# Kernel tuning notes

Measured on AMD Instinct MI355X. Metric: run time of the kernel, lower is better.

## Reference

```python
import jax, jax.numpy as jnp
import numpy as np

EPS = 1e-12  # torch F.normalize default eps

def setup_inputs() -> dict:
    key = jax.random.key(0)
    k1, k2, k3 = jax.random.split(key, 3)
    B, C, H, W = 32, 512, 64, 64
    HEADS = 8
    local_feature = jax.random.normal(k1, (B, C, H, W), dtype=jnp.float32)
    global_feature = jax.random.normal(k2, (B, C, H, W), dtype=jnp.float32)
    temperature = jnp.ones((HEADS, 1, 1), dtype=jnp.float32)
    proj_w = jax.random.normal(k3, (C, C), dtype=jnp.float32) * 0.02  # project_out 1x1 conv weight [out,in]
    return {"local_feature": local_feature, "global_feature": global_feature,
            "temperature": temperature, "proj_w": proj_w}

def _l2norm(x):
    # F.normalize(x, dim=-1): x / max(||x||_2, eps)
    n = jnp.sqrt(jnp.sum(x * x, axis=-1, keepdims=True))
    return x / jnp.maximum(n, EPS)

def reference(local_feature, global_feature, temperature, proj_w):
    B, C, H, W = local_feature.shape
    heads = temperature.shape[0]
    d = C // heads
    split = lambda x: x.reshape(B, heads, d, H * W)  # b (head c) h w -> b head c (hw)
    q = _l2norm(split(local_feature))
    k = _l2norm(split(global_feature))
    v = split(global_feature)
    # channel-attention: [b,h,d,d] score matrix (d small), softmax over last dim
    attn = jax.nn.softmax(jnp.einsum('bhcn,bhdn->bhcd', q, k) * temperature, axis=-1)
    out = jnp.einsum('bhcd,bhdn->bhcn', attn, v).reshape(B, C, H, W)
    # project_out: 1x1 conv, no bias -> channel GEMM
    return jnp.einsum('oc,bchw->bohw', proj_w, out)
```

## Files before the change

kernel.cpp:

```cpp
#include <hip/hip_runtime.h>
#include <stdint.h>

#define B_N 32
#define C_N 512
#define HEADS_N 8
#define D_N 64
#define N_SP 4096

typedef __attribute__((ext_vector_type(8))) short short8;
typedef __attribute__((ext_vector_type(4))) float f32x4;

__device__ __forceinline__ unsigned int f2bf1(float x) {
  unsigned int u = __float_as_uint(x);
  return (u + 0x7fffu + ((u >> 16) & 1u)) >> 16;
}
__device__ __forceinline__ unsigned int packbf(float lo, float hi) {
  return f2bf1(lo) | (f2bf1(hi) << 16);
}

__global__ __launch_bounds__(256) void attn_partial_kernel(
    const float* __restrict__ localf, const float* __restrict__ globf,
    float* __restrict__ pS, float* __restrict__ pssq, int splitk)
{
  const int h = blockIdx.x, b = blockIdx.y, chunk = blockIdx.z;
  const int t = threadIdx.x;
  const int lane = t & 63, w = t >> 6;
  const int rquad = t >> 4;
  const int c4 = t & 15;

  __shared__ unsigned short tA[64 * 72];
  __shared__ unsigned short tB[64 * 72];
  __shared__ float ssqP[2 * 64 * 16];

  const float* Qb = localf + ((size_t)(b * C_N + h * D_N)) * N_SP;
  const float* Kb = globf  + ((size_t)(b * C_N + h * D_N)) * N_SP;

  const int iters = 64 / splitk;
  const int it0 = chunk * iters;

  f32x4 acc[2][2];
#pragma unroll
  for (int i = 0; i < 2; ++i)
#pragma unroll
    for (int j = 0; j < 2; ++j) acc[i][j] = (f32x4){0.f, 0.f, 0.f, 0.f};

  float ssqA[4] = {0.f, 0.f, 0.f, 0.f}, ssqB[4] = {0.f, 0.f, 0.f, 0.f};
  f32x4 qa[4], ka[4];

  {
    int n0 = it0 * 64 + c4 * 4;
#pragma unroll
    for (int i = 0; i < 4; ++i) {
      int row = i * 16 + rquad;
      qa[i] = *(const f32x4*)(Qb + (size_t)row * N_SP + n0);
      ka[i] = *(const f32x4*)(Kb + (size_t)row * N_SP + n0);
    }
  }

  const int lr = lane & 15, lq = lane >> 4;
  const int rbase = (w >> 1) * 32, cbase = (w & 1) * 32;

  for (int it = it0; it < it0 + iters; ++it) {
#pragma unroll
    for (int i = 0; i < 4; ++i) {
      int row = i * 16 + rquad;
      f32x4 q = qa[i], k = ka[i];
      ssqA[i] += q[0]*q[0] + q[1]*q[1] + q[2]*q[2] + q[3]*q[3];
      ssqB[i] += k[0]*k[0] + k[1]*k[1] + k[2]*k[2] + k[3]*k[3];
      uint2 qp; qp.x = packbf(q[0], q[1]); qp.y = packbf(q[2], q[3]);
      uint2 kp; kp.x = packbf(k[0], k[1]); kp.y = packbf(k[2], k[3]);
      *(uint2*)(tA + row * 72 + c4 * 4) = qp;
      *(uint2*)(tB + row * 72 + c4 * 4) = kp;
    }
    __syncthreads();
    if (it + 1 < it0 + iters) {
      int n0 = (it + 1) * 64 + c4 * 4;
#pragma unroll
      for (int i = 0; i < 4; ++i) {
        int row = i * 16 + rquad;
        qa[i] = *(const f32x4*)(Qb + (size_t)row * N_SP + n0);
        ka[i] = *(const f32x4*)(Kb + (size_t)row * N_SP + n0);
      }
    }
#pragma unroll
    for (int s = 0; s < 2; ++s) {
      short8 af[2], bf[2];
#pragma unroll
      for (int mt = 0; mt < 2; ++mt)
        af[mt] = *(const short8*)(tA + (rbase + mt * 16 + lr) * 72 + (s * 4 + lq) * 8);
#pragma unroll
      for (int nt = 0; nt < 2; ++nt)
        bf[nt] = *(const short8*)(tB + (cbase + nt * 16 + lr) * 72 + (s * 4 + lq) * 8);
#pragma unroll
      for (int mt = 0; mt < 2; ++mt)
#pragma unroll
        for (int nt = 0; nt < 2; ++nt)
          acc[mt][nt] = __builtin_amdgcn_mfma_f32_16x16x32_bf16(
              af[mt], bf[nt], acc[mt][nt], 0, 0, 0);
    }
    __syncthreads();
  }

#pragma unroll
  for (int i = 0; i < 4; ++i) {
    ssqP[(0 * 64 + i * 16 + rquad) * 16 + c4] = ssqA[i];
    ssqP[(1 * 64 + i * 16 + rquad) * 16 + c4] = ssqB[i];
  }
  __syncthreads();

  const size_t obase = (size_t)(b * HEADS_N + h) * (size_t)splitk + chunk;
  if (t < 128) {
    int side = t >> 6, row = t & 63;
    float s = 0.f;
#pragma unroll
    for (int j = 0; j < 16; ++j) s += ssqP[(side * 64 + row) * 16 + j];
    pssq[obase * 128 + t] = s;
  }

  float* ps = pS + obase * 4096;
#pragma unroll
  for (int mt = 0; mt < 2; ++mt)
#pragma unroll
    for (int nt = 0; nt < 2; ++nt)
#pragma unroll
      for (int r = 0; r < 4; ++r) {
        int rg = rbase + mt * 16 + lq * 4 + r;
        int cg = cbase + nt * 16 + lr;
        ps[rg * 64 + cg] = acc[mt][nt][r];
      }
}

__global__ __launch_bounds__(256) void attn_combine_kernel(
    const float* __restrict__ pS, const float* __restrict__ pssq,
    const float* __restrict__ temp, float* __restrict__ attn_out, int splitk)
{
  const int h = blockIdx.x, b = blockIdx.y, t = threadIdx.x;
  __shared__ float S[64 * 68];
  __shared__ float invv[128];

  const size_t base = (size_t)(b * HEADS_N + h) * (size_t)splitk;

  float r[16];
#pragma unroll
  for (int i = 0; i < 16; ++i) r[i] = 0.f;
  for (int c = 0; c < splitk; ++c) {
    const float* p = pS + (base + c) * 4096;
#pragma unroll
    for (int i = 0; i < 16; ++i) r[i] += p[t + 256 * i];
  }
  if (t < 128) {
    float s = 0.f;
    for (int c = 0; c < splitk; ++c) s += pssq[(base + c) * 128 + t];
    invv[t] = 1.0f / fmaxf(sqrtf(s), 1e-12f);
  }
#pragma unroll
  for (int i = 0; i < 16; ++i) {
    int e = t + 256 * i;
    S[(e >> 6) * 68 + (e & 63)] = r[i];
  }
  __syncthreads();

  const float tval = temp[h];
#pragma unroll
  for (int i = 0; i < 16; ++i) {
    int e = t + 256 * i;
    int rw = e >> 6, cl = e & 63;
    S[rw * 68 + cl] *= invv[rw] * invv[64 + cl] * tval;
  }
  __syncthreads();

  if (t < 64) {
    float mx = -1e30f;
#pragma unroll 8
    for (int j = 0; j < 64; ++j) mx = fmaxf(mx, S[t * 68 + j]);
    float sum = 0.f;
#pragma unroll 8
    for (int j = 0; j < 64; ++j) {
      float e = __expf(S[t * 68 + j] - mx);
      S[t * 68 + j] = e;
      sum += e;
    }
    float inv = 1.0f / sum;
    float* op = attn_out + ((size_t)((b * HEADS_N + h) * 64 + t)) * 64;
#pragma unroll 8
    for (int j = 0; j < 64; ++j) op[j] = S[t * 68 + j] * inv;
  }
}

__global__ __launch_bounds__(256) void fold_kernel(
    const float* __restrict__ proj, const float* __restrict__ attn,
    unsigned short* __restrict__ Mout)
{
  const int h = blockIdx.x, b = blockIdx.y, zh = blockIdx.z;
  const int t = threadIdx.x;
  __shared__ float A_[64 * 64];
  const float* ap = attn + (size_t)(b * HEADS_N + h) * 4096;
#pragma unroll
  for (int i = 0; i < 16; ++i) A_[i * 256 + t] = ap[i * 256 + t];
  __syncthreads();
  const int e = t & 63, w = t >> 6;
  float col[64];
#pragma unroll
  for (int cc = 0; cc < 64; ++cc) col[cc] = A_[cc * 64 + e];
  unsigned short* mb = Mout + (size_t)b * C_N * C_N + (size_t)h * 64 + e;
  for (int i = 0; i < 16; ++i) {
    int o = zh * 64 + i * 4 + w;
    const float* pr = proj + (size_t)o * C_N + h * 64;
    float s = 0.f;
#pragma unroll
    for (int cc = 0; cc < 64; cc += 4) {
      f32x4 p = *(const f32x4*)(pr + cc);
      s += p[0]*col[cc] + p[1]*col[cc+1] + p[2]*col[cc+2] + p[3]*col[cc+3];
    }
    mb[(size_t)o * C_N] = (unsigned short)f2bf1(s);
  }
}

__global__ __launch_bounds__(256, 2) void final_gemm_kernel(
    const unsigned short* __restrict__ Mw, const float* __restrict__ globf,
    float* __restrict__ outp)
{
  const int nt0 = blockIdx.x;
  const int mt0 = blockIdx.y;
  const int b   = blockIdx.z;
  const int t = threadIdx.x, lane = t & 63, w = t >> 6;
  const int lr = lane & 15, lq = lane >> 4;

  __shared__ unsigned short tA[128 * 72];
  __shared__ unsigned short tB[128 * 72];

  const unsigned short* Mb = Mw + ((size_t)b * C_N + mt0 * 128) * C_N;
  const float* Gb = globf + (size_t)b * C_N * N_SP + nt0 * 128;

  f32x4 acc[4][4];
#pragma unroll
  for (int i = 0; i < 4; ++i)
#pragma unroll
    for (int j = 0; j < 4; ++j) acc[i][j] = (f32x4){0.f, 0.f, 0.f, 0.f};

  const int mq = (w >> 1) * 64, nq2 = (w & 1) * 64;
  const int nq = t & 31, kg = t >> 5;

  int4 av[4];
  f32x4 gv[8];

  {
#pragma unroll
    for (int i = 0; i < 4; ++i) {
      int u = t + 256 * i; int o = u >> 3, j = u & 7;
      av[i] = *(const int4*)(Mb + (size_t)o * C_N + j * 8);
    }
    const float* gp = Gb + (size_t)(kg * 8) * N_SP + nq * 4;
#pragma unroll
    for (int i = 0; i < 8; ++i) gv[i] = *(const f32x4*)(gp + (size_t)i * N_SP);
  }

  for (int kb = 0; kb < 8; ++kb) {
#pragma unroll
    for (int i = 0; i < 4; ++i) {
      int u = t + 256 * i; int o = u >> 3, j = u & 7;
      *(int4*)(tA + o * 72 + j * 8) = av[i];
    }
#pragma unroll
    for (int r = 0; r < 4; ++r) {
      int n = nq * 4 + r;
      int4 pk;
      pk.x = (int)packbf(gv[0][r], gv[1][r]);
      pk.y = (int)packbf(gv[2][r], gv[3][r]);
      pk.z = (int)packbf(gv[4][r], gv[5][r]);
      pk.w = (int)packbf(gv[6][r], gv[7][r]);
      int gph = kg ^ (nq & 7);
      *(int4*)(tB + n * 72 + gph * 8) = pk;
    }
    __syncthreads();
    if (kb < 7) {
      int kn = (kb + 1) * 64;
#pragma unroll
      for (int i = 0; i < 4; ++i) {
        int u = t + 256 * i; int o = u >> 3, j = u & 7;
        av[i] = *(const int4*)(Mb + (size_t)o * C_N + kn + j * 8);
      }
      const float* gp = Gb + (size_t)(kn + kg * 8) * N_SP + nq * 4;
#pragma unroll
      for (int i = 0; i < 8; ++i) gv[i] = *(const f32x4*)(gp + (size_t)i * N_SP);
    }
#pragma unroll
    for (int s = 0; s < 2; ++s) {
      short8 af[4], bf[4];
#pragma unroll
      for (int mt = 0; mt < 4; ++mt)
        af[mt] = *(const short8*)(tA + (mq + mt * 16 + lr) * 72 + (s * 4 + lq) * 8);
#pragma unroll
      for (int nt = 0; nt < 4; ++nt) {
        int n = nq2 + nt * 16 + lr;
        int g2 = (s * 4 + lq) ^ ((n >> 2) & 7);
        bf[nt] = *(const short8*)(tB + n * 72 + g2 * 8);
      }
#pragma unroll
      for (int mt = 0; mt < 4; ++mt)
#pragma unroll
        for (int nt = 0; nt < 4; ++nt)
          acc[mt][nt] = __builtin_amdgcn_mfma_f32_16x16x32_bf16(
              af[mt], bf[nt], acc[mt][nt], 0, 0, 0);
    }
    __syncthreads();
  }

  float* ob = outp + ((size_t)(b * C_N + mt0 * 128 + mq)) * N_SP + nt0 * 128 + nq2;
#pragma unroll
  for (int mt = 0; mt < 4; ++mt)
#pragma unroll
    for (int nt = 0; nt < 4; ++nt)
#pragma unroll
      for (int r = 0; r < 4; ++r)
        ob[(size_t)(mt * 16 + lq * 4 + r) * N_SP + nt * 16 + lr] = acc[mt][nt][r];
}

extern "C" void kernel_launch(void* const* d_in, const int* in_sizes, int n_in,
                              void* d_out, int out_size, void* d_ws, size_t ws_size,
                              hipStream_t stream) {
  const float* localf = (const float*)d_in[0];
  const float* globf  = (const float*)d_in[1];
  const float* temp   = (const float*)d_in[2];
  const float* proj   = (const float*)d_in[3];
  float* out = (float*)d_out;

  const size_t ATTN_BYTES = (size_t)B_N * HEADS_N * 64 * 64 * sizeof(float);
  const size_t M_BYTES    = (size_t)B_N * C_N * C_N * sizeof(unsigned short);

  int splitk = 8;
  while (splitk > 1) {
    size_t need = ATTN_BYTES + M_BYTES +
                  (size_t)B_N * HEADS_N * (size_t)splitk * (4096 + 128) * sizeof(float);
    if (need <= ws_size) break;
    splitk >>= 1;
  }

  float* attn_ws = (float*)d_ws;
  unsigned short* M_ws = (unsigned short*)((char*)d_ws + ATTN_BYTES);
  float* pS   = (float*)((char*)d_ws + ATTN_BYTES + M_BYTES);
  float* pssq = pS + (size_t)B_N * HEADS_N * (size_t)splitk * 4096;

  attn_partial_kernel<<<dim3(HEADS_N, B_N, splitk), 256, 0, stream>>>(
      localf, globf, pS, pssq, splitk);
  attn_combine_kernel<<<dim3(HEADS_N, B_N), 256, 0, stream>>>(
      pS, pssq, temp, attn_ws, splitk);
  fold_kernel<<<dim3(HEADS_N, B_N, 8), 256, 0, stream>>>(proj, attn_ws, M_ws);
  final_gemm_kernel<<<dim3(32, 4, B_N), 256, 0, stream>>>(M_ws, globf, out);
}
```

Baseline: 951.7 us.

## Stage GEMM epilogue through LDS for vectorized stores; shuffle-reduce ssq; raise occupancy

The final GEMM epilogue now writes each 16-row accumulator slice into shared memory and reads it back so every thread issues 16-byte row-contiguous global stores, replacing scattered scalar stores. The partial-attention kernel replaces its shared-memory sum-of-squares reduction and barrier with a warp shuffle-xor reduction. Launch bounds are raised on both kernels to request higher occupancy. The extra barriers in the epilogue and tighter register limits could add stalls or spills.

```diff
diff --git a/kernel.cpp b/kernel.cpp
--- a/kernel.cpp
+++ b/kernel.cpp
@@ -18,7 +18,7 @@
   return f2bf1(lo) | (f2bf1(hi) << 16);
 }
 
-__global__ __launch_bounds__(256) void attn_partial_kernel(
+__global__ __launch_bounds__(256, 6) void attn_partial_kernel(
     const float* __restrict__ localf, const float* __restrict__ globf,
     float* __restrict__ pS, float* __restrict__ pssq, int splitk)
 {
@@ -30,7 +30,6 @@
 
   __shared__ unsigned short tA[64 * 72];
   __shared__ unsigned short tB[64 * 72];
-  __shared__ float ssqP[2 * 64 * 16];
 
   const float* Qb = localf + ((size_t)(b * C_N + h * D_N)) * N_SP;
   const float* Kb = globf  + ((size_t)(b * C_N + h * D_N)) * N_SP;
@@ -101,20 +100,21 @@
     __syncthreads();
   }
 
+  const size_t obase = (size_t)(b * HEADS_N + h) * (size_t)splitk + chunk;
+
 #pragma unroll
   for (int i = 0; i < 4; ++i) {
-    ssqP[(0 * 64 + i * 16 + rquad) * 16 + c4] = ssqA[i];
-    ssqP[(1 * 64 + i * 16 + rquad) * 16 + c4] = ssqB[i];
-  }
-  __syncthreads();
-
-  const size_t obase = (size_t)(b * HEADS_N + h) * (size_t)splitk + chunk;
-  if (t < 128) {
-    int side = t >> 6, row = t & 63;
-    float s = 0.f;
-#pragma unroll
-    for (int j = 0; j < 16; ++j) s += ssqP[(side * 64 + row) * 16 + j];
-    pssq[obase * 128 + t] = s;
+    float a = ssqA[i], bb = ssqB[i];
+#pragma unroll
+    for (int m = 8; m >= 1; m >>= 1) {
+      a  += __shfl_xor(a, m, 64);
+      bb += __shfl_xor(bb, m, 64);
+    }
+    if (c4 == 0) {
+      int row = i * 16 + rquad;
+      pssq[obase * 128 + row]      = a;
+      pssq[obase * 128 + 64 + row] = bb;
+    }
   }
 
   float* ps = pS + obase * 4096;
@@ -216,7 +216,7 @@
   }
 }
 
-__global__ __launch_bounds__(256, 2) void final_gemm_kernel(
+__global__ __launch_bounds__(256, 4) void final_gemm_kernel(
     const unsigned short* __restrict__ Mw, const float* __restrict__ globf,
     float* __restrict__ outp)
 {
@@ -306,14 +306,26 @@
     __syncthreads();
   }
 
-  float* ob = outp + ((size_t)(b * C_N + mt0 * 128 + mq)) * N_SP + nt0 * 128 + nq2;
-#pragma unroll
-  for (int mt = 0; mt < 4; ++mt)
+  float* E = (float*)tA;
+  float* E_w = E + w * (16 * 68);
+#pragma unroll
+  for (int mt = 0; mt < 4; ++mt) {
+    __syncthreads();
 #pragma unroll
     for (int nt = 0; nt < 4; ++nt)
 #pragma unroll
       for (int r = 0; r < 4; ++r)
-        ob[(size_t)(mt * 16 + lq * 4 + r) * N_SP + nt * 16 + lr] = acc[mt][nt][r];
+        E_w[(lq * 4 + r) * 68 + nt * 16 + lr] = acc[mt][nt][r];
+    __syncthreads();
+    float* ob = outp + ((size_t)(b * C_N + mt0 * 128 + mq + mt * 16)) * N_SP
+              + nt0 * 128 + nq2;
+#pragma unroll
+    for (int rr = 0; rr < 4; ++rr) {
+      int row = rr * 4 + lq;
+      f32x4 v = *(const f32x4*)(E_w + row * 68 + lr * 4);
+      *(f32x4*)(ob + (size_t)row * N_SP + lr * 4) = v;
+    }
+  }
 }
 
 extern "C" void kernel_launch(void* const* d_in, const int* in_sizes, int n_in,
```

After: 1.047 ms. 1.1x slower.
